# Performance work log

Hardware: AMD Instinct MI355X
Metric: run time of the kernel (lower is better)

## Reference

```python
import jax, jax.numpy as jnp
import numpy as np

CUTOFF = 5.0
N_RBF = 20
N_NODES, N_EDGES, F = 50000, 200000, 128


def setup_inputs() -> dict:
    key = jax.random.key(0)
    ks = jax.random.split(key, 11)
    inp = {
        "s": jax.random.normal(ks[0], (N_NODES, F), jnp.float32),
        "v": jax.random.normal(ks[1], (N_NODES, 3, F), jnp.float32),
        "rel_pos": jax.random.normal(ks[2], (N_EDGES, 3), jnp.float32),
        "W1": jax.random.normal(ks[3], (F, F), jnp.float32) * 0.05,
        "b1": jnp.zeros((F,), jnp.float32),
        "W2": jax.random.normal(ks[4], (F, 3 * F), jnp.float32) * 0.05,
        "b2": jnp.zeros((3 * F,), jnp.float32),
        "Wr": jax.random.normal(ks[5], (N_RBF, 3 * F), jnp.float32) * 0.05,
        "br": jnp.zeros((3 * F,), jnp.float32),
        "src": jax.random.randint(ks[6], (N_EDGES,), 0, N_NODES),
        "dst": jax.random.randint(ks[7], (N_EDGES,), 0, N_NODES),
    }
    return inp


def reference(s, v, rel_pos, W1, b1, W2, b2, Wr, br, src, dst):
    n_nodes, f = s.shape
    # phi MLP on node scalar features (computed per node, then gathered per edge)
    phi = jax.nn.silu(s @ W1 + b1) @ W2 + b2          # [N, 3F]
    phi_e = phi[src]                                   # [E, 3F]

    d = jnp.linalg.norm(rel_pos, axis=-1)              # [E]
    # sinc-style radial basis: sin(n*pi*d/cutoff)/d, n = 1..N_RBF
    n = jnp.arange(1, N_RBF + 1, dtype=d.dtype)
    rbf = jnp.sin(n * (jnp.pi / CUTOFF) * d[:, None]) / d[:, None]  # [E, 20]
    w_proj = rbf @ Wr + br                             # [E, 3F]
    # cosine cutoff gate
    fcut = 0.5 * (jnp.cos(jnp.pi * d / CUTOFF) + 1.0) * (d < CUTOFF)
    w = w_proj * fcut[:, None]                         # [E, 3F]

    split = w * phi_e                                  # hadamard gate, [E, 3F]
    s_v, s_s, s_r = split[:, :f], split[:, f:2 * f], split[:, 2 * f:]

    dirv = rel_pos / d[:, None]                        # r / ||r||, [E, 3]
    # vector message: gated neighbor vectors + gated directions
    dv = v[src] * s_v[:, None, :] + dirv[:, :, None] * s_r[:, None, :]  # [E,3,F]

    out_s = jax.ops.segment_sum(s_s, dst, num_segments=n_nodes)  # [N, F]
    out_v = jax.ops.segment_sum(dv, dst, num_segments=n_nodes)   # [N, 3, F]
    return out_v, out_s
```

## Files before the change

kernel.cpp:

```cpp
#include <hip/hip_runtime.h>
#include <math.h>

#define N_NODES_C 50000
#define N_EDGES_C 200000
#define FDIM 128
#define NRBF 20
#define CUT 5.0f
#define SC_BLK 196
#define GBLOCKS 4096
#define BATCH 32

typedef short  bf16x8 __attribute__((ext_vector_type(8)));
typedef float  f32x4  __attribute__((ext_vector_type(4)));
typedef _Float16 f16x2 __attribute__((ext_vector_type(2)));

__device__ __forceinline__ unsigned short f32_to_bf16(float f) {
    unsigned u = __float_as_uint(f);
    unsigned r = (u + 0x7FFFu + ((u >> 16) & 1u)) >> 16;
    return (unsigned short)r;
}
__device__ __forceinline__ float bf16_to_f32(unsigned short h) {
    return __uint_as_float(((unsigned)h) << 16);
}
__device__ __forceinline__ unsigned short f16_bits(float x) {
    _Float16 h = (_Float16)x;
    unsigned short b;
    __builtin_memcpy(&b, &h, 2);
    return b;
}
__device__ __forceinline__ f16x2 u2h2(unsigned u) {
    f16x2 r;
    __builtin_memcpy(&r, &u, 4);
    return r;
}
__device__ __forceinline__ bf16x8 pack_bf16x8(float4 a, float4 b) {
    bf16x8 r;
    r[0] = (short)f32_to_bf16(a.x); r[1] = (short)f32_to_bf16(a.y);
    r[2] = (short)f32_to_bf16(a.z); r[3] = (short)f32_to_bf16(a.w);
    r[4] = (short)f32_to_bf16(b.x); r[5] = (short)f32_to_bf16(b.y);
    r[6] = (short)f32_to_bf16(b.z); r[7] = (short)f32_to_bf16(b.w);
    return r;
}

__global__ __launch_bounds__(256) void prep_w_kernel(
    const float* __restrict__ W1, const float* __restrict__ W2,
    unsigned short* __restrict__ W1t, unsigned short* __restrict__ W2t)
{
    int i = blockIdx.x * 256 + threadIdx.x;
    if (i < 128 * 128) {
        int n = i >> 7, k = i & 127;
        W1t[i] = f32_to_bf16(W1[k * 128 + n]);
    }
    int j = i - 128 * 128;
    if (j >= 0 && j < 384 * 128) {
        int n = j >> 7, k = j & 127;
        W2t[j] = f32_to_bf16(W2[k * 384 + n]);
    }
}

__global__ __launch_bounds__(256) void prep_wr_kernel(
    const float* __restrict__ Wr, unsigned* __restrict__ wrh)
{
    int idx = blockIdx.x * 256 + threadIdx.x;
    if (idx >= 128 * 30) return;
    int f  = idx / 30;
    int r  = idx % 30;
    int sec = r / 10, kp = r % 10;
    int col = sec * 128 + f;
    unsigned lo = f16_bits(Wr[(2 * kp)     * 384 + col]);
    unsigned hi = f16_bits(Wr[(2 * kp + 1) * 384 + col]);
    wrh[idx] = lo | (hi << 16);
}

__global__ __launch_bounds__(256) void mlp1w_kernel(
    const float* __restrict__ s, const unsigned short* __restrict__ W1t,
    const float* __restrict__ b1, unsigned short* __restrict__ h)
{
    __shared__ unsigned short w1lds[128 * 136];

    const int tid = threadIdx.x;
#pragma unroll
    for (int j = 0; j < 8; ++j) {
        int fi = tid + j * 256;
        int row  = fi >> 4;
        int colq = fi & 15;
        *(float4*)&w1lds[row * 136 + colq * 8] =
            *(const float4*)(W1t + (size_t)fi * 8);
    }
    __syncthreads();

    const int wv = tid >> 6, lane = tid & 63;
    const int m0 = blockIdx.x * 64 + wv * 16;
    const int lr = lane & 15, lg = lane >> 4;
    int arow = m0 + lr; if (arow >= N_NODES_C) arow = N_NODES_C - 1;

    f32x4 acc[8];
#pragma unroll
    for (int nt = 0; nt < 8; ++nt) acc[nt] = (f32x4){0.f, 0.f, 0.f, 0.f};

#pragma unroll
    for (int kt = 0; kt < 4; ++kt) {
        const int k0 = kt * 32 + lg * 8;
        const float4* ap = (const float4*)(s + (size_t)arow * 128 + k0);
        bf16x8 af = pack_bf16x8(ap[0], ap[1]);
#pragma unroll
        for (int nt = 0; nt < 8; ++nt) {
            bf16x8 bf = *(const bf16x8*)&w1lds[(nt * 16 + lr) * 136 + k0];
            acc[nt] = __builtin_amdgcn_mfma_f32_16x16x32_bf16(af, bf, acc[nt], 0, 0, 0);
        }
    }

    const int crow = m0 + lg * 4;
#pragma unroll
    for (int nt = 0; nt < 8; ++nt) {
        int col = nt * 16 + lr;
        float bb = b1[col];
#pragma unroll
        for (int r = 0; r < 4; ++r) {
            int m = crow + r;
            if (m < N_NODES_C) {
                float x = acc[nt][r] + bb;
                x = x / (1.f + __expf(-x));
                h[(size_t)m * 128 + col] = f32_to_bf16(x);
            }
        }
    }
}

__global__ __launch_bounds__(256) void mlp2pv_kernel(
    const unsigned short* __restrict__ h, const unsigned short* __restrict__ W2t,
    const float* __restrict__ b2, const float* __restrict__ v,
    unsigned short* __restrict__ pv)
{
    __shared__ unsigned short wlds[3 * 16 * 136];

    const int tid = threadIdx.x;
    const int wv = tid >> 6, lane = tid & 63;
    const int m0 = blockIdx.x * 64 + wv * 16;
    const int lr = lane & 15, lg = lane >> 4;
    int arow = m0 + lr; if (arow >= N_NODES_C) arow = N_NODES_C - 1;

    bf16x8 af2[4];
#pragma unroll
    for (int kt = 0; kt < 4; ++kt)
        af2[kt] = *(const bf16x8*)(h + (size_t)arow * 128 + kt * 32 + lg * 8);

    const int crow = m0 + lg * 4;

    for (int nt = 0; nt < 8; ++nt) {
        __syncthreads();
#pragma unroll
        for (int j = 0; j < 3; ++j) {
            int fi = tid + j * 256;
            int c    = fi >> 8;
            int rem  = fi & 255;
            int row  = rem >> 4;
            int colq = rem & 15;
            *(float4*)&wlds[(c * 16 + row) * 136 + colq * 8] =
                *(const float4*)(W2t +
                    ((size_t)(c * 128 + nt * 16 + row) * 128 + colq * 8));
        }
        __syncthreads();

        f32x4 a0 = (f32x4){0.f, 0.f, 0.f, 0.f};
        f32x4 a1 = (f32x4){0.f, 0.f, 0.f, 0.f};
        f32x4 a2 = (f32x4){0.f, 0.f, 0.f, 0.f};
#pragma unroll
        for (int kt = 0; kt < 4; ++kt) {
            const int k0 = kt * 32 + lg * 8;
            bf16x8 bf0 = *(const bf16x8*)&wlds[(      lr) * 136 + k0];
            bf16x8 bf1 = *(const bf16x8*)&wlds[(16 +  lr) * 136 + k0];
            bf16x8 bf2 = *(const bf16x8*)&wlds[(32 +  lr) * 136 + k0];
            a0 = __builtin_amdgcn_mfma_f32_16x16x32_bf16(af2[kt], bf0, a0, 0, 0, 0);
            a1 = __builtin_amdgcn_mfma_f32_16x16x32_bf16(af2[kt], bf1, a1, 0, 0, 0);
            a2 = __builtin_amdgcn_mfma_f32_16x16x32_bf16(af2[kt], bf2, a2, 0, 0, 0);
        }

        const int col = nt * 16 + lr;
        const float bb0 = b2[col], bb1 = b2[128 + col], bb2 = b2[256 + col];
#pragma unroll
        for (int r = 0; r < 4; ++r) {
            int m = crow + r;
            if (m < N_NODES_C) {
                const float* vr = v + (size_t)m * 384;
                unsigned p0 = f32_to_bf16(a0[r] + bb0);
                unsigned p1 = f32_to_bf16(a1[r] + bb1);
                unsigned p2 = f32_to_bf16(a2[r] + bb2);
                unsigned v0 = f32_to_bf16(vr[col]);
                unsigned v1 = f32_to_bf16(vr[128 + col]);
                unsigned v2 = f32_to_bf16(vr[256 + col]);
                uint4 val;
                val.x = p0 | (p1 << 16);
                val.y = p2 | (v0 << 16);
                val.z = v1 | (v2 << 16);
                val.w = 0;
                *(uint4*)((char*)pv + (size_t)m * 2048 + (size_t)col * 16) = val;
            }
        }
    }
}

__global__ __launch_bounds__(256) void count_kernel(
    const int* __restrict__ dst, int* __restrict__ counts)
{
    int e = blockIdx.x * 256 + threadIdx.x;
    if (e < N_EDGES_C) atomicAdd(counts + dst[e], 1);
}

__global__ __launch_bounds__(256) void scan1_kernel(
    const int* __restrict__ counts, int* __restrict__ row_tmp,
    int* __restrict__ partial)
{
    __shared__ int sm[256];
    const int t = threadIdx.x;
    const int idx = blockIdx.x * 256 + t;
    int c = (idx < N_NODES_C) ? counts[idx] : 0;
    int x = c;
    sm[t] = x;
    __syncthreads();
#pragma unroll
    for (int off = 1; off < 256; off <<= 1) {
        int y = (t >= off) ? sm[t - off] : 0;
        __syncthreads();
        x += y;
        sm[t] = x;
        __syncthreads();
    }
    if (idx < N_NODES_C) row_tmp[idx] = x - c;
    if (t == 255) partial[blockIdx.x] = x;
}

__global__ __launch_bounds__(256) void scan2_kernel(
    const int* __restrict__ partial, int* __restrict__ poffs)
{
    __shared__ int sm[256];
    const int t = threadIdx.x;
    int c = (t < SC_BLK) ? partial[t] : 0;
    int x = c;
    sm[t] = x;
    __syncthreads();
#pragma unroll
    for (int off = 1; off < 256; off <<= 1) {
        int y = (t >= off) ? sm[t - off] : 0;
        __syncthreads();
        x += y;
        sm[t] = x;
        __syncthreads();
    }
    if (t < SC_BLK) poffs[t] = x - c;
}

__global__ __launch_bounds__(256) void scan3_kernel(
    const int* __restrict__ row_tmp, const int* __restrict__ poffs,
    int* __restrict__ row_ptr, int* __restrict__ row_fill)
{
    const int idx = blockIdx.x * 256 + threadIdx.x;
    if (idx < N_NODES_C) {
        int rp = row_tmp[idx] + poffs[blockIdx.x];
        row_ptr[idx]  = rp;
        row_fill[idx] = rp;
    }
    if (idx == 0) row_ptr[N_NODES_C] = N_EDGES_C;
}

__global__ __launch_bounds__(256) void fill_kernel(
    const float* __restrict__ rel_pos, const int* __restrict__ src,
    const int* __restrict__ dst, int* __restrict__ row_fill,
    float* __restrict__ e_meta)
{
    int e = blockIdx.x * 256 + threadIdx.x;
    if (e >= N_EDGES_C) return;

    int pos = atomicAdd(row_fill + dst[e], 1);

    float x = rel_pos[3 * e + 0];
    float y = rel_pos[3 * e + 1];
    float z = rel_pos[3 * e + 2];
    float d = sqrtf(x * x + y * y + z * z);
    float invd = 1.0f / d;

    float s1 = 0.f, c1 = 0.f, fcut = 0.f, amp = 0.f;
    if (d < CUT) {
        sincosf((3.14159265358979f / CUT) * d, &s1, &c1);
        fcut = 0.5f * (c1 + 1.0f);
        amp  = invd * fcut;
    }

    float rb[NRBF];
    float sk = s1, ck = c1;
#pragma unroll
    for (int k = 0; k < NRBF; ++k) {
        rb[k] = sk * amp;
        float sn = sk * c1 + ck * s1;
        ck = ck * c1 - sk * s1;
        sk = sn;
    }

    unsigned pk[10];
#pragma unroll
    for (int kp = 0; kp < 10; ++kp)
        pk[kp] = (unsigned)f16_bits(rb[2 * kp]) | ((unsigned)f16_bits(rb[2 * kp + 1]) << 16);

    float4* mp = (float4*)(e_meta + (size_t)pos * 16);
    mp[0] = make_float4(x * invd, y * invd, z * invd, fcut);
    mp[1] = make_float4(__uint_as_float(pk[0]), __uint_as_float(pk[1]),
                        __uint_as_float(pk[2]), __uint_as_float(pk[3]));
    mp[2] = make_float4(__uint_as_float(pk[4]), __uint_as_float(pk[5]),
                        __uint_as_float(pk[6]), __uint_as_float(pk[7]));
    mp[3] = make_float4(__uint_as_float(pk[8]), __uint_as_float(pk[9]),
                        __int_as_float(src[e]), 0.f);
}

#define COMPUTE_E(M_, U)                                                       \
    {                                                                          \
        const float4 m0 = *(const float4*)(M_);                                \
        const unsigned* mu_ = (const unsigned*)((M_) + 4);                     \
        float w0 = m0.w * br0, w1 = m0.w * br1, w2 = m0.w * br2;               \
        _Pragma("unroll")                                                      \
        for (int kp = 0; kp < 10; ++kp) {                                      \
            f16x2 rh = u2h2(mu_[kp]);                                          \
            w0 = __builtin_amdgcn_fdot2(rh, u2h2(wrp0[kp]), w0, false);        \
            w1 = __builtin_amdgcn_fdot2(rh, u2h2(wrp1[kp]), w1, false);        \
            w2 = __builtin_amdgcn_fdot2(rh, u2h2(wrp2[kp]), w2, false);        \
        }                                                                      \
        float P0 = bf16_to_f32((unsigned short)((U).x & 0xFFFFu));             \
        float P1 = bf16_to_f32((unsigned short)((U).x >> 16));                 \
        float P2 = bf16_to_f32((unsigned short)((U).y & 0xFFFFu));             \
        float V0 = bf16_to_f32((unsigned short)((U).y >> 16));                 \
        float V1 = bf16_to_f32((unsigned short)((U).z & 0xFFFFu));             \
        float V2 = bf16_to_f32((unsigned short)((U).z >> 16));                 \
        float sv = w0 * P0;                                                    \
        float ss = w1 * P1;                                                    \
        float sr = w2 * P2;                                                    \
        acc_s  += ss;                                                          \
        acc_v0 += V0 * sv + m0.x * sr;                                         \
        acc_v1 += V1 * sv + m0.y * sr;                                         \
        acc_v2 += V2 * sv + m0.z * sr;                                         \
    }

#define LOADPV(U, SI)                                                          \
    U = *(const uint4*)((const char*)pv + (size_t)(SI) * 2048 + (size_t)f * 16);

#define STORE_NODE(N_, AS, A0, A1, A2)                                         \
    {                                                                          \
        out_s[(size_t)(N_) * 128 + f] = AS;                                    \
        out_v[(size_t)(N_) * 384 +       f] = A0;                              \
        out_v[(size_t)(N_) * 384 + 128 + f] = A1;                              \
        out_v[(size_t)(N_) * 384 + 256 + f] = A2;                              \
    }

#define BOUNDARY(GE)                                                           \
    if ((GE) + 1 == end_cur) {                                                 \
        STORE_NODE(cur, acc_s, acc_v0, acc_v1, acc_v2);                        \
        acc_s = acc_v0 = acc_v1 = acc_v2 = 0.f;                                \
        ++cur;                                                                 \
        while (cur < nhi) {                                                    \
            int ne_ = row_ptr[cur + 1];                                        \
            if (ne_ != (GE) + 1) { end_cur = ne_; break; }                     \
            STORE_NODE(cur, 0.f, 0.f, 0.f, 0.f);                               \
            ++cur;                                                             \
        }                                                                      \
    }

__global__ __launch_bounds__(128) void gather_packed_kernel(
    const unsigned short* __restrict__ pv, const unsigned* __restrict__ wrh,
    const float* __restrict__ br, const int* __restrict__ row_ptr,
    const float* __restrict__ e_meta,
    float* __restrict__ out_v, float* __restrict__ out_s)
{
    __shared__ float meta_lds[2][BATCH * 16];

    const int f = threadIdx.x;
    const int gid = blockIdx.x;
    const int chunk = (N_NODES_C + GBLOCKS - 1) / GBLOCKS;
    const int nlo = gid * chunk;
    if (nlo >= N_NODES_C) return;
    const int nhi = min(nlo + chunk, N_NODES_C);

    unsigned wrp0[10], wrp1[10], wrp2[10];
    {
        const unsigned* wp = wrh + (size_t)f * 30;
#pragma unroll
        for (int i = 0; i < 10; ++i) {
            wrp0[i] = wp[i];
            wrp1[i] = wp[10 + i];
            wrp2[i] = wp[20 + i];
        }
#pragma unroll
        for (int i = 0; i < 10; ++i)
            asm volatile("" : "+v"(wrp0[i]), "+v"(wrp1[i]), "+v"(wrp2[i]));
    }
    const float br0 = br[f], br1 = br[128 + f], br2 = br[256 + f];

    const int gbeg = row_ptr[nlo];
    const int gend = row_ptr[nhi];
    const int nedge = gend - gbeg;

    float acc_s = 0.f, acc_v0 = 0.f, acc_v1 = 0.f, acc_v2 = 0.f;

    int cur = nlo;
    while (cur < nhi && row_ptr[cur + 1] == gbeg) {
        STORE_NODE(cur, 0.f, 0.f, 0.f, 0.f);
        ++cur;
    }
    int end_cur = (cur < nhi) ? row_ptr[cur + 1] : gbeg;

    if (nedge > 0) {
        const float4* src0 = (const float4*)(e_meta + (size_t)gbeg * 16);
        ((float4*)meta_lds[0])[threadIdx.x] = src0[threadIdx.x];
    }
    __syncthreads();

    const int total_batches = (nedge + BATCH - 1) / BATCH;
    for (int b = 0; b < total_batches; ++b) {
        const int bstart = b * BATCH;
        const int bcount = min(BATCH, nedge - bstart);
        const bool have_next = (b + 1 < total_batches);

        float4 st;
        if (have_next)
            st = ((const float4*)(e_meta + (size_t)(gbeg + bstart + BATCH) * 16))[threadIdx.x];

        const float* Mb = meta_lds[b & 1];

        uint4 uA, uB;
        {
            int si = ((const int*)Mb)[14];
            LOADPV(uA, si);
        }

        int t = 0;
        while (t < bcount) {
            if (t + 1 < bcount) {
                int si = ((const int*)(Mb + (t + 1) * 16))[14];
                LOADPV(uB, si);
            }
            COMPUTE_E(Mb + t * 16, uA);
            BOUNDARY(gbeg + bstart + t);
            ++t; if (t >= bcount) break;

            if (t + 1 < bcount) {
                int si = ((const int*)(Mb + (t + 1) * 16))[14];
                LOADPV(uA, si);
            }
            COMPUTE_E(Mb + t * 16, uB);
            BOUNDARY(gbeg + bstart + t);
            ++t;
        }

        if (have_next) ((float4*)meta_lds[(b + 1) & 1])[threadIdx.x] = st;
        __syncthreads();
    }
}

extern "C" void kernel_launch(void* const* d_in, const int* in_sizes, int n_in,
                              void* d_out, int out_size, void* d_ws, size_t ws_size,
                              hipStream_t stream)
{
    const float* s  = (const float*)d_in[0];
    const float* v  = (const float*)d_in[1];
    const float* rp = (const float*)d_in[2];
    const float* W1 = (const float*)d_in[3];
    const float* b1 = (const float*)d_in[4];
    const float* W2 = (const float*)d_in[5];
    const float* b2 = (const float*)d_in[6];
    const float* Wr = (const float*)d_in[7];
    const float* br = (const float*)d_in[8];
    const int* src  = (const int*)d_in[9];
    const int* dst  = (const int*)d_in[10];

    float* out   = (float*)d_out;
    float* out_v = out;
    float* out_s = out + (size_t)N_NODES_C * 3 * FDIM;

    char* ws = (char*)d_ws;
    float* e_meta = (float*)ws;                 ws += ((size_t)N_EDGES_C * 16 + 256) * sizeof(float);
    unsigned short* W1t = (unsigned short*)ws;  ws += (size_t)128 * 128 * sizeof(unsigned short);
    unsigned short* W2t = (unsigned short*)ws;  ws += (size_t)384 * 128 * sizeof(unsigned short);
    unsigned* wrh = (unsigned*)ws;              ws += (size_t)128 * 30 * sizeof(unsigned);
    int* counts   = (int*)ws;                   ws += (size_t)N_NODES_C * sizeof(int);
    int* row_ptr  = (int*)ws;                   ws += (size_t)(N_NODES_C + 4) * sizeof(int);
    int* row_fill = (int*)ws;                   ws += (size_t)N_NODES_C * sizeof(int);
    int* row_tmp  = (int*)ws;                   ws += (size_t)N_NODES_C * sizeof(int);
    int* partial  = (int*)ws;                   ws += (size_t)256 * sizeof(int);
    int* poffs    = (int*)ws;                   ws += (size_t)256 * sizeof(int);
    unsigned short* h = (unsigned short*)ws;    ws += (size_t)N_NODES_C * 128 * sizeof(unsigned short);
    unsigned short* pv = (unsigned short*)ws;

    hipMemsetAsync(counts, 0, (size_t)N_NODES_C * sizeof(int), stream);

    count_kernel<<<(N_EDGES_C + 255) / 256, 256, 0, stream>>>(dst, counts);
    scan1_kernel<<<SC_BLK, 256, 0, stream>>>(counts, row_tmp, partial);
    scan2_kernel<<<1, 256, 0, stream>>>(partial, poffs);
    scan3_kernel<<<SC_BLK, 256, 0, stream>>>(row_tmp, poffs, row_ptr, row_fill);
    fill_kernel<<<(N_EDGES_C + 255) / 256, 256, 0, stream>>>(rp, src, dst, row_fill, e_meta);

    prep_w_kernel<<<256, 256, 0, stream>>>(W1, W2, W1t, W2t);
    prep_wr_kernel<<<15, 256, 0, stream>>>(Wr, wrh);
    mlp1w_kernel<<<(N_NODES_C + 63) / 64, 256, 0, stream>>>(s, W1t, b1, h);
    mlp2pv_kernel<<<(N_NODES_C + 63) / 64, 256, 0, stream>>>(h, W2t, b2, v, pv);

    gather_packed_kernel<<<GBLOCKS, 128, 0, stream>>>(pv, wrh, br, row_ptr,
                                                      e_meta, out_v, out_s);
}
```

Before: 228.8 us.

## Pack pv to 12 bytes, double-buffer W2 LDS tiles, raise gather block count

Shrinks the per-node-feature packed phi/v record from 16 to 12 bytes by dropping the unused padding word. This cuts the memory footprint and gather traffic of the per-edge pv loads in the aggregation kernel. Separately, the MLP2 kernel now double-buffers its W2 tile in LDS, prefetching the next slice into registers during the MFMAs and needing one barrier per iteration. The gather grid size is also raised from 4096 to 6250 blocks. Risks are that the 12-byte accesses are not 16-byte aligned, so loads may split, and that the extra blocks add per-block overhead.

```diff
diff --git a/kernel.cpp b/kernel.cpp
--- a/kernel.cpp
+++ b/kernel.cpp
@@ -7,11 +7,12 @@
 #define NRBF 20
 #define CUT 5.0f
 #define SC_BLK 196
-#define GBLOCKS 4096
+#define GBLOCKS 6250
 #define BATCH 32
 
 typedef short  bf16x8 __attribute__((ext_vector_type(8)));
 typedef float  f32x4  __attribute__((ext_vector_type(4)));
+typedef unsigned int u32x3 __attribute__((ext_vector_type(3)));
 typedef _Float16 f16x2 __attribute__((ext_vector_type(2)));
 
 __device__ __forceinline__ unsigned short f32_to_bf16(float f) {
@@ -132,7 +133,7 @@
     const float* __restrict__ b2, const float* __restrict__ v,
     unsigned short* __restrict__ pv)
 {
-    __shared__ unsigned short wlds[3 * 16 * 136];
+    __shared__ unsigned short wlds[2][3 * 16 * 136];
 
     const int tid = threadIdx.x;
     const int wv = tid >> 6, lane = tid & 63;
@@ -145,32 +146,44 @@
     for (int kt = 0; kt < 4; ++kt)
         af2[kt] = *(const bf16x8*)(h + (size_t)arow * 128 + kt * 32 + lg * 8);
 
+    const int fi0 = tid, fi1 = tid + 256, fi2 = tid + 512;
+#define SLICE_SRC(FI, NT)                                                      \
+    (const float4*)(W2t + ((size_t)(((FI) >> 8) * 128 + (NT) * 16 +            \
+                            (((FI) & 255) >> 4)) * 128 + ((FI) & 15) * 8))
+#define SLICE_DST(BUF, FI)                                                     \
+    (float4*)&wlds[BUF][(((FI) >> 8) * 16 + (((FI) & 255) >> 4)) * 136 +       \
+                        ((FI) & 15) * 8]
+
+    {
+        float4 r0 = *SLICE_SRC(fi0, 0);
+        float4 r1 = *SLICE_SRC(fi1, 0);
+        float4 r2 = *SLICE_SRC(fi2, 0);
+        *SLICE_DST(0, fi0) = r0;
+        *SLICE_DST(0, fi1) = r1;
+        *SLICE_DST(0, fi2) = r2;
+    }
+    __syncthreads();
+
     const int crow = m0 + lg * 4;
 
     for (int nt = 0; nt < 8; ++nt) {
-        __syncthreads();
-#pragma unroll
-        for (int j = 0; j < 3; ++j) {
-            int fi = tid + j * 256;
-            int c    = fi >> 8;
-            int rem  = fi & 255;
-            int row  = rem >> 4;
-            int colq = rem & 15;
-            *(float4*)&wlds[(c * 16 + row) * 136 + colq * 8] =
-                *(const float4*)(W2t +
-                    ((size_t)(c * 128 + nt * 16 + row) * 128 + colq * 8));
-        }
-        __syncthreads();
-
+        float4 r0, r1, r2;
+        if (nt + 1 < 8) {
+            r0 = *SLICE_SRC(fi0, nt + 1);
+            r1 = *SLICE_SRC(fi1, nt + 1);
+            r2 = *SLICE_SRC(fi2, nt + 1);
+        }
+
+        const unsigned short* W = wlds[nt & 1];
         f32x4 a0 = (f32x4){0.f, 0.f, 0.f, 0.f};
         f32x4 a1 = (f32x4){0.f, 0.f, 0.f, 0.f};
         f32x4 a2 = (f32x4){0.f, 0.f, 0.f, 0.f};
 #pragma unroll
         for (int kt = 0; kt < 4; ++kt) {
             const int k0 = kt * 32 + lg * 8;
-            bf16x8 bf0 = *(const bf16x8*)&wlds[(      lr) * 136 + k0];
-            bf16x8 bf1 = *(const bf16x8*)&wlds[(16 +  lr) * 136 + k0];
-            bf16x8 bf2 = *(const bf16x8*)&wlds[(32 +  lr) * 136 + k0];
+            bf16x8 bf0 = *(const bf16x8*)&W[(      lr) * 136 + k0];
+            bf16x8 bf1 = *(const bf16x8*)&W[(16 +  lr) * 136 + k0];
+            bf16x8 bf2 = *(const bf16x8*)&W[(32 +  lr) * 136 + k0];
             a0 = __builtin_amdgcn_mfma_f32_16x16x32_bf16(af2[kt], bf0, a0, 0, 0, 0);
             a1 = __builtin_amdgcn_mfma_f32_16x16x32_bf16(af2[kt], bf1, a1, 0, 0, 0);
             a2 = __builtin_amdgcn_mfma_f32_16x16x32_bf16(af2[kt], bf2, a2, 0, 0, 0);
@@ -189,15 +202,23 @@
                 unsigned v0 = f32_to_bf16(vr[col]);
                 unsigned v1 = f32_to_bf16(vr[128 + col]);
                 unsigned v2 = f32_to_bf16(vr[256 + col]);
-                uint4 val;
+                u32x3 val;
                 val.x = p0 | (p1 << 16);
                 val.y = p2 | (v0 << 16);
                 val.z = v1 | (v2 << 16);
-                val.w = 0;
-                *(uint4*)((char*)pv + (size_t)m * 2048 + (size_t)col * 16) = val;
+                *(u32x3*)((char*)pv + (size_t)m * 1536 + (size_t)col * 12) = val;
             }
         }
-    }
+
+        if (nt + 1 < 8) {
+            *SLICE_DST((nt + 1) & 1, fi0) = r0;
+            *SLICE_DST((nt + 1) & 1, fi1) = r1;
+            *SLICE_DST((nt + 1) & 1, fi2) = r2;
+        }
+        __syncthreads();
+    }
+#undef SLICE_SRC
+#undef SLICE_DST
 }
 
 __global__ __launch_bounds__(256) void count_kernel(
@@ -339,7 +360,7 @@
     }
 
 #define LOADPV(U, SI)                                                          \
-    U = *(const uint4*)((const char*)pv + (size_t)(SI) * 2048 + (size_t)f * 16);
+    U = *(const u32x3*)((const char*)pv + (size_t)(SI) * 1536 + (size_t)f * 12);
 
 #define STORE_NODE(N_, AS, A0, A1, A2)                                         \
     {                                                                          \
@@ -423,7 +444,7 @@
 
         const float* Mb = meta_lds[b & 1];
 
-        uint4 uA, uB;
+        u32x3 uA, uB;
         {
             int si = ((const int*)Mb)[14];
             LOADPV(uA, si);
```

New measurement: 205.3 us. 10.3% less time.

## Shrink packed node record to 12 bytes, merge prep kernels, retune gather grid

Applied to the files above, without the earlier changes.

The per-node packed phi/v record drops its padding word, going from 16 to 12 bytes per feature. This reduces the memory footprint and gather traffic of the per-edge random reads. The two weight-prep kernels are merged into one launch. mlp2pv now handles 32 rows per block with waves split across the two column halves. The gather kernel gets more blocks, an occupancy hint of 5 in launch_bounds, and volatile weight loads in place of the asm register pinning. The 12-byte loads may compile into less efficient split accesses, and the occupancy hint may cause register spills.

```diff
diff --git a/kernel.cpp b/kernel.cpp
--- a/kernel.cpp
+++ b/kernel.cpp
@@ -7,11 +7,12 @@
 #define NRBF 20
 #define CUT 5.0f
 #define SC_BLK 196
-#define GBLOCKS 4096
+#define GBLOCKS 6250
 #define BATCH 32
 
 typedef short  bf16x8 __attribute__((ext_vector_type(8)));
 typedef float  f32x4  __attribute__((ext_vector_type(4)));
+typedef unsigned int u32x3 __attribute__((ext_vector_type(3)));
 typedef _Float16 f16x2 __attribute__((ext_vector_type(2)));
 
 __device__ __forceinline__ unsigned short f32_to_bf16(float f) {
@@ -42,34 +43,31 @@
     return r;
 }
 
-__global__ __launch_bounds__(256) void prep_w_kernel(
+__global__ __launch_bounds__(256) void prep_all_kernel(
     const float* __restrict__ W1, const float* __restrict__ W2,
-    unsigned short* __restrict__ W1t, unsigned short* __restrict__ W2t)
+    const float* __restrict__ Wr, unsigned short* __restrict__ W1t,
+    unsigned short* __restrict__ W2t, unsigned* __restrict__ wrh)
 {
     int i = blockIdx.x * 256 + threadIdx.x;
     if (i < 128 * 128) {
         int n = i >> 7, k = i & 127;
         W1t[i] = f32_to_bf16(W1[k * 128 + n]);
-    }
-    int j = i - 128 * 128;
-    if (j >= 0 && j < 384 * 128) {
+    } else if (i < 128 * 128 + 384 * 128) {
+        int j = i - 128 * 128;
         int n = j >> 7, k = j & 127;
         W2t[j] = f32_to_bf16(W2[k * 384 + n]);
-    }
-}
-
-__global__ __launch_bounds__(256) void prep_wr_kernel(
-    const float* __restrict__ Wr, unsigned* __restrict__ wrh)
-{
-    int idx = blockIdx.x * 256 + threadIdx.x;
-    if (idx >= 128 * 30) return;
-    int f  = idx / 30;
-    int r  = idx % 30;
-    int sec = r / 10, kp = r % 10;
-    int col = sec * 128 + f;
-    unsigned lo = f16_bits(Wr[(2 * kp)     * 384 + col]);
-    unsigned hi = f16_bits(Wr[(2 * kp + 1) * 384 + col]);
-    wrh[idx] = lo | (hi << 16);
+    } else {
+        int idx = i - (128 * 128 + 384 * 128);
+        if (idx < 128 * 30) {
+            int f  = idx / 30;
+            int r  = idx % 30;
+            int sec = r / 10, kp = r % 10;
+            int col = sec * 128 + f;
+            unsigned lo = f16_bits(Wr[(2 * kp)     * 384 + col]);
+            unsigned hi = f16_bits(Wr[(2 * kp + 1) * 384 + col]);
+            wrh[idx] = lo | (hi << 16);
+        }
+    }
 }
 
 __global__ __launch_bounds__(256) void mlp1w_kernel(
@@ -132,11 +130,13 @@
     const float* __restrict__ b2, const float* __restrict__ v,
     unsigned short* __restrict__ pv)
 {
-    __shared__ unsigned short wlds[3 * 16 * 136];
+    __shared__ unsigned short wlds[2][3 * 16 * 136];
 
     const int tid = threadIdx.x;
     const int wv = tid >> 6, lane = tid & 63;
-    const int m0 = blockIdx.x * 64 + wv * 16;
+    const int rg = wv & 1;
+    const int hf = wv >> 1;
+    const int m0 = blockIdx.x * 32 + rg * 16;
     const int lr = lane & 15, lg = lane >> 4;
     int arow = m0 + lr; if (arow >= N_NODES_C) arow = N_NODES_C - 1;
 
@@ -147,36 +147,40 @@
 
     const int crow = m0 + lg * 4;
 
-    for (int nt = 0; nt < 8; ++nt) {
-        __syncthreads();
-#pragma unroll
-        for (int j = 0; j < 3; ++j) {
+    for (int t = 0; t < 4; ++t) {
+        __syncthreads();
+#pragma unroll
+        for (int j = 0; j < 6; ++j) {
             int fi = tid + j * 256;
-            int c    = fi >> 8;
-            int rem  = fi & 255;
-            int row  = rem >> 4;
-            int colq = rem & 15;
-            *(float4*)&wlds[(c * 16 + row) * 136 + colq * 8] =
+            int half = (fi >= 768) ? 1 : 0;
+            int rem  = fi - half * 768;
+            int c    = rem >> 8;
+            int r2   = rem & 255;
+            int row  = r2 >> 4;
+            int colq = r2 & 15;
+            int nt   = half * 4 + t;
+            *(float4*)&wlds[half][(c * 16 + row) * 136 + colq * 8] =
                 *(const float4*)(W2t +
                     ((size_t)(c * 128 + nt * 16 + row) * 128 + colq * 8));
         }
         __syncthreads();
 
+        const unsigned short* W = wlds[hf];
         f32x4 a0 = (f32x4){0.f, 0.f, 0.f, 0.f};
         f32x4 a1 = (f32x4){0.f, 0.f, 0.f, 0.f};
         f32x4 a2 = (f32x4){0.f, 0.f, 0.f, 0.f};
 #pragma unroll
         for (int kt = 0; kt < 4; ++kt) {
             const int k0 = kt * 32 + lg * 8;
-            bf16x8 bf0 = *(const bf16x8*)&wlds[(      lr) * 136 + k0];
-            bf16x8 bf1 = *(const bf16x8*)&wlds[(16 +  lr) * 136 + k0];
-            bf16x8 bf2 = *(const bf16x8*)&wlds[(32 +  lr) * 136 + k0];
+            bf16x8 bf0 = *(const bf16x8*)&W[(      lr) * 136 + k0];
+            bf16x8 bf1 = *(const bf16x8*)&W[(16 +  lr) * 136 + k0];
+            bf16x8 bf2 = *(const bf16x8*)&W[(32 +  lr) * 136 + k0];
             a0 = __builtin_amdgcn_mfma_f32_16x16x32_bf16(af2[kt], bf0, a0, 0, 0, 0);
             a1 = __builtin_amdgcn_mfma_f32_16x16x32_bf16(af2[kt], bf1, a1, 0, 0, 0);
             a2 = __builtin_amdgcn_mfma_f32_16x16x32_bf16(af2[kt], bf2, a2, 0, 0, 0);
         }
 
-        const int col = nt * 16 + lr;
+        const int col = (hf * 4 + t) * 16 + lr;
         const float bb0 = b2[col], bb1 = b2[128 + col], bb2 = b2[256 + col];
 #pragma unroll
         for (int r = 0; r < 4; ++r) {
@@ -189,12 +193,11 @@
                 unsigned v0 = f32_to_bf16(vr[col]);
                 unsigned v1 = f32_to_bf16(vr[128 + col]);
                 unsigned v2 = f32_to_bf16(vr[256 + col]);
-                uint4 val;
+                u32x3 val;
                 val.x = p0 | (p1 << 16);
                 val.y = p2 | (v0 << 16);
                 val.z = v1 | (v2 << 16);
-                val.w = 0;
-                *(uint4*)((char*)pv + (size_t)m * 2048 + (size_t)col * 16) = val;
+                *(u32x3*)((char*)pv + (size_t)m * 1536 + (size_t)col * 12) = val;
             }
         }
     }
@@ -339,7 +342,7 @@
     }
 
 #define LOADPV(U, SI)                                                          \
-    U = *(const uint4*)((const char*)pv + (size_t)(SI) * 2048 + (size_t)f * 16);
+    U = *(const u32x3*)((const char*)pv + (size_t)(SI) * 1536 + (size_t)f * 12);
 
 #define STORE_NODE(N_, AS, A0, A1, A2)                                         \
     {                                                                          \
@@ -362,7 +365,7 @@
         }                                                                      \
     }
 
-__global__ __launch_bounds__(128) void gather_packed_kernel(
+__global__ __launch_bounds__(128, 5) void gather_packed_kernel(
     const unsigned short* __restrict__ pv, const unsigned* __restrict__ wrh,
     const float* __restrict__ br, const int* __restrict__ row_ptr,
     const float* __restrict__ e_meta,
@@ -379,16 +382,13 @@
 
     unsigned wrp0[10], wrp1[10], wrp2[10];
     {
-        const unsigned* wp = wrh + (size_t)f * 30;
+        volatile const unsigned* wp = wrh + (size_t)f * 30;
 #pragma unroll
         for (int i = 0; i < 10; ++i) {
             wrp0[i] = wp[i];
             wrp1[i] = wp[10 + i];
             wrp2[i] = wp[20 + i];
         }
-#pragma unroll
-        for (int i = 0; i < 10; ++i)
-            asm volatile("" : "+v"(wrp0[i]), "+v"(wrp1[i]), "+v"(wrp2[i]));
     }
     const float br0 = br[f], br1 = br[128 + f], br2 = br[256 + f];
 
@@ -423,7 +423,7 @@
 
         const float* Mb = meta_lds[b & 1];
 
-        uint4 uA, uB;
+        u32x3 uA, uB;
         {
             int si = ((const int*)Mb)[14];
             LOADPV(uA, si);
@@ -495,10 +495,9 @@
     scan3_kernel<<<SC_BLK, 256, 0, stream>>>(row_tmp, poffs, row_ptr, row_fill);
     fill_kernel<<<(N_EDGES_C + 255) / 256, 256, 0, stream>>>(rp, src, dst, row_fill, e_meta);
 
-    prep_w_kernel<<<256, 256, 0, stream>>>(W1, W2, W1t, W2t);
-    prep_wr_kernel<<<15, 256, 0, stream>>>(Wr, wrh);
+    prep_all_kernel<<<272, 256, 0, stream>>>(W1, W2, Wr, W1t, W2t, wrh);
     mlp1w_kernel<<<(N_NODES_C + 63) / 64, 256, 0, stream>>>(s, W1t, b1, h);
-    mlp2pv_kernel<<<(N_NODES_C + 63) / 64, 256, 0, stream>>>(h, W2t, b2, v, pv);
+    mlp2pv_kernel<<<(N_NODES_C + 31) / 32, 256, 0, stream>>>(h, W2t, b2, v, pv);
 
     gather_packed_kernel<<<GBLOCKS, 128, 0, stream>>>(pv, wrh, br, row_ptr,
                                                       e_meta, out_v, out_s);
```

After: 281.8 us. +23.2%, slower.
